# Optimization experiments

Measured on AMD Instinct MI355X. Metric: run time of the kernel, lower is better.

Reference implementation:

```python
import jax, jax.numpy as jnp
import numpy as np

N_OBJ, N_P, N2 = 16, 128, 2048
C, H, W = 256, 384, 384
IMG_W, IMG_H = 384.0, 384.0  # img_metas['img_shape'][:2][::-1]
SIM_THR = 0.0
LOSS_WEIGHT = 1.0
COS_EPS = 1e-8  # torch F.cosine_similarity default


def setup_inputs() -> dict:
    key = jax.random.key(0)
    k1, k2, k3, k4 = jax.random.split(key, 4)
    img_size = jnp.array([IMG_W, IMG_H], jnp.float32)
    point_set_1 = jax.random.uniform(k1, (N_OBJ, N_P, 2), jnp.float32) * img_size
    point_set_2 = jax.random.uniform(k2, (N_OBJ, N2, 2), jnp.float32) * img_size
    key_points = jax.random.uniform(k3, (N_OBJ * N_P, 2), jnp.float32) * img_size
    feats = jax.random.normal(k4, (1, C, H, W), jnp.float32)
    return {"point_set_1": point_set_1, "point_set_2": point_set_2,
            "feats": feats, "key_points": key_points}


def _grid_sample(img, pts01):
    # img: [C,H,W]; pts01: [P,2] (x,y) in [0,1]. Bilinear, align_corners=False,
    # zero padding -- matches mmcv point_sample / torch grid_sample.
    Ci, Hi, Wi = img.shape
    g = 2.0 * pts01 - 1.0
    x = ((g[:, 0] + 1.0) * Wi - 1.0) * 0.5
    y = ((g[:, 1] + 1.0) * Hi - 1.0) * 0.5
    x0 = jnp.floor(x)
    y0 = jnp.floor(y)
    wx1 = x - x0
    wy1 = y - y0

    def tap(xi, yi, wgt):
        valid = (xi >= 0) & (xi < Wi) & (yi >= 0) & (yi < Hi)
        xc = jnp.clip(xi, 0, Wi - 1).astype(jnp.int32)
        yc = jnp.clip(yi, 0, Hi - 1).astype(jnp.int32)
        return img[:, yc, xc] * (wgt * valid)[None, :]  # [C,P]

    return (tap(x0, y0, (1 - wx1) * (1 - wy1))
            + tap(x0 + 1, y0, wx1 * (1 - wy1))
            + tap(x0, y0 + 1, (1 - wx1) * wy1)
            + tap(x0 + 1, y0 + 1, wx1 * wy1))  # [C,P]


def reference(point_set_1, point_set_2, feats, key_points):
    img_size = jnp.array([IMG_W, IMG_H], feats.dtype)
    img = feats[0]  # feats.expand() reuses the same map for every object

    # feats_set_1: [n_obj, n_p, C]; feats_set_2: [n_obj, n2, C]
    f1 = _grid_sample(img, key_points / img_size).T.reshape(N_OBJ, N_P, C)
    f2 = _grid_sample(img, (point_set_2 / img_size).reshape(-1, 2)).T.reshape(N_OBJ, N2, C)

    # cosine similarity over channel dim (norms clamped to eps like torch)
    n1 = jnp.maximum(jnp.linalg.norm(f1, axis=-1), COS_EPS)  # [O,P]
    n2 = jnp.maximum(jnp.linalg.norm(f2, axis=-1), COS_EPS)  # [O,N2]
    sims = jnp.einsum('opc,onc->opn', f1, f2) / (n1[..., None] * n2[:, None, :])
    mask = sims >= SIM_THR  # [O,P,N2]

    # pairwise L2 distances between each key point and candidate set
    diff = point_set_1[:, :, None, :] - point_set_2[:, None, :, :]
    d = jnp.linalg.norm(diff, axis=-1)  # [O,P,N2]

    cnt = mask.sum(-1)  # [O,P]
    has = cnt > 0
    dmin = jnp.min(jnp.where(mask, d, jnp.inf), axis=-1)
    dmean = jnp.sum(jnp.where(mask, d, 0.0), axis=-1) / jnp.maximum(cnt, 1)
    # chamfer of a single point vs masked set: (nearest + mean)/2, 'mean' reduction
    m = (point_set_2.sum(axis=(1, 2)) >= 0).astype(d.dtype)  # [O]
    cost = jnp.where(has, 0.5 * (dmin + dmean), 0.0) * m[:, None]  # [O,P]

    dist = (cost.sum(-1) / N_P).mean()
    return dist * LOSS_WEIGHT
```

## Files before the change

### kernel.cpp

```cpp
#include <hip/hip_runtime.h>
#include <hip/hip_bf16.h>
#include <math.h>

#define W_    384
#define H_    384
#define HW_   (384*384)
#define C_    256
#define NOBJ  16
#define NP    128
#define N2    2048
#define NF1   (NOBJ*NP)
#define NPTS  (NOBJ*NP + NOBJ*N2)
#define NG    16
#define NT    8

#define TX    63
#define TY    8
#define NTX   7
#define NTY   48
#define NTILE (NTX*NTY)
#define CAP   256
#define CCH   32
#define DXP   68
#define CST   (9*DXP)

typedef __attribute__((ext_vector_type(8))) short short8;
typedef __attribute__((ext_vector_type(4))) float f32x4;

__device__ __forceinline__ unsigned short f2bf(float v) {
    unsigned int u = __float_as_uint(v);
    u += 0x7fffu + ((u >> 16) & 1u);
    return (unsigned short)(u >> 16);
}
__device__ __forceinline__ float bf2f(unsigned short s) {
    return __uint_as_float((unsigned)s << 16);
}

__device__ __forceinline__ void patch_setup(float px, float py,
                                            int& ixb, int& iyb,
                                            float& w00, float& w01,
                                            float& w10, float& w11) {
    float x = px - 0.5f, y = py - 0.5f;
    float xf = floorf(x), yf = floorf(y);
    int ix0 = (int)xf, iy0 = (int)yf;
    float fx = x - xf, fy = y - yf;
    ixb = min(max(ix0, 0), W_ - 2);
    iyb = min(max(iy0, 0), H_ - 2);
    float wA = (ix0 < 0) ? fx : ((ix0 >= W_ - 1) ? 0.f : 1.f - fx);
    float wB = (ix0 < 0) ? 0.f : ((ix0 >= W_ - 1) ? 1.f - fx : fx);
    float uA = (iy0 < 0) ? fy : ((iy0 >= H_ - 1) ? 0.f : 1.f - fy);
    float uB = (iy0 < 0) ? 0.f : ((iy0 >= H_ - 1) ? 1.f - fy : fy);
    w00 = uA * wA; w01 = uA * wB; w10 = uB * wA; w11 = uB * wB;
}

__global__ __launch_bounds__(256) void k_bin(const float* __restrict__ kpts,
                                             const float* __restrict__ ps2,
                                             int* __restrict__ counts,
                                             float4* __restrict__ list) {
    int p = blockIdx.x * 256 + threadIdx.x;
    const float* src = (p < NF1) ? (kpts + (size_t)p * 2)
                                 : (ps2 + (size_t)(p - NF1) * 2);
    float px = src[0], py = src[1];
    int ixb, iyb; float w00, w01, w10, w11;
    patch_setup(px, py, ixb, iyb, w00, w01, w10, w11);
    int tile = (iyb >> 3) * NTX + ixb / TX;
    int slot = atomicAdd(&counts[tile], 1);
    if (slot < CAP) {
        float4 e; e.x = px; e.y = py; e.z = __int_as_float(p); e.w = 0.f;
        list[tile * CAP + slot] = e;
    }
}

__global__ __launch_bounds__(256) void k_gather(const float* __restrict__ feats,
                                                const int* __restrict__ counts,
                                                const float4* __restrict__ list,
                                                unsigned short* __restrict__ f12) {
    __shared__ unsigned short lds[CCH * CST];
    int b    = blockIdx.x;
    int tile = b >> 3;
    int cq   = b & 7;
    int ty = tile / NTX, tx = tile - ty * NTX;
    int x0 = tx * TX, y0 = ty * TY;
    int t  = threadIdx.x;
    int cb = cq * CCH;
    bool edge = (tx == NTX - 1);

    #pragma unroll
    for (int half = 0; half < 2; ++half) {
        int id  = half * 256 + t;
        int c   = id >> 4;
        int dx4 = (id & 15) * 4;
        const float* cbase = feats + (size_t)(cb + c) * HW_;
        unsigned short* ldst = &lds[c * CST + dx4];
        #pragma unroll
        for (int dy = 0; dy < 9; ++dy) {
            int yy = min(y0 + dy, H_ - 1);
            float4 v;
            if (!edge) {
                v = *(const float4*)(cbase + yy * W_ + x0 + dx4);
            } else {
                const float* rowp = cbase + yy * W_;
                v.x = rowp[min(x0 + dx4 + 0, W_ - 1)];
                v.y = rowp[min(x0 + dx4 + 1, W_ - 1)];
                v.z = rowp[min(x0 + dx4 + 2, W_ - 1)];
                v.w = rowp[min(x0 + dx4 + 3, W_ - 1)];
            }
            ushort4 pk;
            pk.x = f2bf(v.x); pk.y = f2bf(v.y); pk.z = f2bf(v.z); pk.w = f2bf(v.w);
            *(ushort4*)(ldst + dy * DXP) = pk;
        }
    }
    __syncthreads();

    int cnt  = min(counts[tile], CAP);
    int lane = t & 63, wave = t >> 6;
    int sub  = lane >> 2;
    int g    = lane & 3;

    for (int i = wave * 16 + sub; i < cnt; i += 64) {
        float4 e = list[tile * CAP + i];
        int point = __float_as_int(e.z);
        int ixb, iyb; float w00, w01, w10, w11;
        patch_setup(e.x, e.y, ixb, iyb, w00, w01, w10, w11);
        int dxb = ixb - x0, dyb = iyb - y0;

        unsigned short u[8];
        #pragma unroll
        for (int j = 0; j < 8; ++j) {
            const unsigned short* base = &lds[(g * 8 + j) * CST + dyb * DXP + dxb];
            float v = w00 * bf2f(base[0])   + w01 * bf2f(base[1])
                    + w10 * bf2f(base[DXP]) + w11 * bf2f(base[DXP + 1]);
            u[j] = f2bf(v);
        }
        uint4 pk;
        pk.x = (unsigned)u[0] | ((unsigned)u[1] << 16);
        pk.y = (unsigned)u[2] | ((unsigned)u[3] << 16);
        pk.z = (unsigned)u[4] | ((unsigned)u[5] << 16);
        pk.w = (unsigned)u[6] | ((unsigned)u[7] << 16);
        *(uint4*)(f12 + (size_t)point * C_ + cb + g * 8) = pk;
    }
}

__global__ __launch_bounds__(256) void k_simdist(const unsigned short* __restrict__ f12,
                                                 const float* __restrict__ ps1,
                                                 const float* __restrict__ ps2,
                                                 float* __restrict__ pmin,
                                                 float* __restrict__ psum,
                                                 float* __restrict__ pcnt) {
    int wid  = blockIdx.x * 4 + (threadIdx.x >> 6);
    int lane = threadIdx.x & 63;
    int ng = wid & 15;
    int pt = (wid >> 4) & 7;
    int o  = wid >> 7;
    int quad = lane >> 4, col = lane & 15;

    const short* f12s = (const short*)f12;
    const short8* aptr =
        (const short8*)(f12s + ((size_t)(o * NP + pt * 16 + col) * C_ + quad * 8));
    short8 a[8];
    #pragma unroll
    for (int kb = 0; kb < 8; ++kb) a[kb] = aptr[kb * 4];

    const float2* ps1v = (const float2*)ps1;
    const float2* ps2v = (const float2*)ps2;
    float pxr[4], pyr[4];
    #pragma unroll
    for (int r = 0; r < 4; ++r) {
        float2 pc = ps1v[o * NP + pt * 16 + quad * 4 + r];
        pxr[r] = pc.x; pyr[r] = pc.y;
    }

    float mn[4] = {INFINITY, INFINITY, INFINITY, INFINITY};
    float sm[4] = {0.f, 0.f, 0.f, 0.f};
    float ct[4] = {0.f, 0.f, 0.f, 0.f};

    for (int t = 0; t < NT; ++t) {
        int nbase = ng * 128 + t * 16;
        const short8* bptr =
            (const short8*)(f12s + ((size_t)(NF1 + o * N2 + nbase + col) * C_ + quad * 8));
        f32x4 acc = {0.f, 0.f, 0.f, 0.f};
        #pragma unroll
        for (int kb = 0; kb < 8; ++kb)
            acc = __builtin_amdgcn_mfma_f32_16x16x32_bf16(a[kb], bptr[kb * 4], acc, 0, 0, 0);

        float2 nc = ps2v[o * N2 + nbase + col];
        #pragma unroll
        for (int r = 0; r < 4; ++r) {
            if (acc[r] >= 0.f) {
                float dx = pxr[r] - nc.x, dy = pyr[r] - nc.y;
                float d  = sqrtf(dx * dx + dy * dy);
                mn[r] = fminf(mn[r], d); sm[r] += d; ct[r] += 1.f;
            }
        }
    }

    #pragma unroll
    for (int r = 0; r < 4; ++r) {
        #pragma unroll
        for (int off = 1; off < 16; off <<= 1) {
            mn[r] = fminf(mn[r], __shfl_xor(mn[r], off, 16));
            sm[r] += __shfl_xor(sm[r], off, 16);
            ct[r] += __shfl_xor(ct[r], off, 16);
        }
    }
    if (col == 0) {
        #pragma unroll
        for (int r = 0; r < 4; ++r) {
            int p   = pt * 16 + quad * 4 + r;
            int idx = (o * NP + p) * NG + ng;
            pmin[idx] = mn[r]; psum[idx] = sm[r]; pcnt[idx] = ct[r];
        }
    }
}

__global__ __launch_bounds__(1024) void k_final(const float* __restrict__ pmin,
                                                const float* __restrict__ psum,
                                                const float* __restrict__ pcnt,
                                                float* __restrict__ out) {
    int t = threadIdx.x;
    float tot = 0.f;
    for (int pair = t; pair < NOBJ * NP; pair += 1024) {
        int base = pair * NG;
        const float4* pm = (const float4*)(pmin + base);
        const float4* ps = (const float4*)(psum + base);
        const float4* pc = (const float4*)(pcnt + base);
        float mn = INFINITY, sm = 0.f, ct = 0.f;
        #pragma unroll
        for (int g4 = 0; g4 < 4; ++g4) {
            float4 a = pm[g4], bq = ps[g4], c = pc[g4];
            mn = fminf(mn, fminf(fminf(a.x, a.y), fminf(a.z, a.w)));
            sm += bq.x + bq.y + bq.z + bq.w;
            ct += c.x + c.y + c.z + c.w;
        }
        if (ct > 0.f) tot += 0.5f * (mn + sm / ct);
    }
    #pragma unroll
    for (int off = 32; off; off >>= 1) tot += __shfl_xor(tot, off, 64);
    __shared__ float wsum[16];
    if ((t & 63) == 0) wsum[t >> 6] = tot;
    __syncthreads();
    if (t < 64) {
        float v = (t < 16) ? wsum[t] : 0.f;
        #pragma unroll
        for (int off = 8; off; off >>= 1) v += __shfl_xor(v, off, 16);
        if (t == 0) out[0] = v * (1.0f / (NOBJ * NP));
    }
}

extern "C" void kernel_launch(void* const* d_in, const int* in_sizes, int n_in,
                              void* d_out, int out_size, void* d_ws, size_t ws_size,
                              hipStream_t stream) {
    const float* ps1   = (const float*)d_in[0];
    const float* ps2   = (const float*)d_in[1];
    const float* feats = (const float*)d_in[2];
    const float* kpts  = (const float*)d_in[3];
    float* out = (float*)d_out;

    const size_t sz_f12  = (size_t)NPTS * C_ * sizeof(unsigned short);
    const size_t sz_part = (size_t)NOBJ * NP * NG * sizeof(float);
    const size_t sz_cnt  = (size_t)NTILE * sizeof(int);
    const size_t sz_cnt_pad = 4096;

    char* ws = (char*)d_ws;
    unsigned short* f12 = (unsigned short*)ws;
    float*  pmin = (float*) (ws + sz_f12);
    float*  psum = (float*) (ws + sz_f12 + sz_part);
    float*  pcnt = (float*) (ws + sz_f12 + 2 * sz_part);
    int*    cnts = (int*)   (ws + sz_f12 + 3 * sz_part);
    float4* list = (float4*)(ws + sz_f12 + 3 * sz_part + sz_cnt_pad);

    hipMemsetAsync(cnts, 0, sz_cnt, stream);
    k_bin<<<NPTS / 256, 256, 0, stream>>>(kpts, ps2, cnts, list);
    k_gather<<<NTILE * 8, 256, 0, stream>>>(feats, cnts, list, f12);
    k_simdist<<<NOBJ * 8 * NG / 4, 256, 0, stream>>>(f12, ps1, ps2, pmin, psum, pcnt);
    k_final<<<1, 1024, 0, stream>>>(pmin, psum, pcnt, out);
}
```

Baseline: 290.7 us.

## Restructure tile gather: smaller channel chunks, fp32 LDS, batched row loads

The tile-staging gather kernel now handles 16 channels per block instead of 32, which doubles the grid and sets launch bounds for 4 blocks per CU. Each thread issues all nine float4 row loads into registers before writing any of them to LDS. Tiles are stored in LDS as fp32, so the bf16 round-trip during staging and the bf16 decode during interpolation both go away. The edge-column special case is replaced by a clamped linear index that may read into the next row; those columns are never used in interpolation. The intent is more memory-level parallelism on the feature-map read, in exchange for narrower 8-byte output stores and more blocks re-reading the halo rows.

Result: faster. 276.5 us (-4.9%).

```diff
diff --git a/kernel.cpp b/kernel.cpp
--- a/kernel.cpp
+++ b/kernel.cpp
@@ -20,9 +20,7 @@
 #define NTY   48
 #define NTILE (NTX*NTY)
 #define CAP   256
-#define CCH   32
-#define DXP   68
-#define CST   (9*DXP)
+#define CCH   16
 
 typedef __attribute__((ext_vector_type(8))) short short8;
 typedef __attribute__((ext_vector_type(4))) float f32x4;
@@ -31,9 +29,6 @@
     unsigned int u = __float_as_uint(v);
     u += 0x7fffu + ((u >> 16) & 1u);
     return (unsigned short)(u >> 16);
-}
-__device__ __forceinline__ float bf2f(unsigned short s) {
-    return __uint_as_float((unsigned)s << 16);
 }
 
 __device__ __forceinline__ void patch_setup(float px, float py,
@@ -71,44 +66,36 @@
     }
 }
 
-__global__ __launch_bounds__(256) void k_gather(const float* __restrict__ feats,
-                                                const int* __restrict__ counts,
-                                                const float4* __restrict__ list,
-                                                unsigned short* __restrict__ f12) {
-    __shared__ unsigned short lds[CCH * CST];
+__global__ __launch_bounds__(256, 4) void k_gather(const float* __restrict__ feats,
+                                                   const int* __restrict__ counts,
+                                                   const float4* __restrict__ list,
+                                                   unsigned short* __restrict__ f12) {
+    __shared__ float lds[9 * 16 * 64];
     int b    = blockIdx.x;
-    int tile = b >> 3;
-    int cq   = b & 7;
+    int tile = b >> 4;
+    int cq   = b & 15;
+    int cb   = cq * CCH;
     int ty = tile / NTX, tx = tile - ty * NTX;
     int x0 = tx * TX, y0 = ty * TY;
     int t  = threadIdx.x;
-    int cb = cq * CCH;
-    bool edge = (tx == NTX - 1);
-
-    #pragma unroll
-    for (int half = 0; half < 2; ++half) {
-        int id  = half * 256 + t;
-        int c   = id >> 4;
-        int dx4 = (id & 15) * 4;
-        const float* cbase = feats + (size_t)(cb + c) * HW_;
-        unsigned short* ldst = &lds[c * CST + dx4];
+
+    {
+        int c   = t >> 4;
+        int dx4 = (t & 15) * 4;
+        size_t cgbase = (size_t)(cb + c) * HW_ + x0 + dx4;
+        const size_t LIM = (size_t)HW_ * C_ - 4;
+        float4 r[9];
         #pragma unroll
         for (int dy = 0; dy < 9; ++dy) {
             int yy = min(y0 + dy, H_ - 1);
-            float4 v;
-            if (!edge) {
-                v = *(const float4*)(cbase + yy * W_ + x0 + dx4);
-            } else {
-                const float* rowp = cbase + yy * W_;
-                v.x = rowp[min(x0 + dx4 + 0, W_ - 1)];
-                v.y = rowp[min(x0 + dx4 + 1, W_ - 1)];
-                v.z = rowp[min(x0 + dx4 + 2, W_ - 1)];
-                v.w = rowp[min(x0 + dx4 + 3, W_ - 1)];
-            }
-            ushort4 pk;
-            pk.x = f2bf(v.x); pk.y = f2bf(v.y); pk.z = f2bf(v.z); pk.w = f2bf(v.w);
-            *(ushort4*)(ldst + dy * DXP) = pk;
-        }
+            size_t gidx = cgbase + (size_t)yy * W_;
+            gidx = gidx > LIM ? LIM : gidx;
+            r[dy] = *(const float4*)(feats + gidx);
+        }
+        float* ldst = &lds[c * 64 + dx4];
+        #pragma unroll
+        for (int dy = 0; dy < 9; ++dy)
+            *(float4*)(ldst + dy * 1024) = r[dy];
     }
     __syncthreads();
 
@@ -123,21 +110,20 @@
         int ixb, iyb; float w00, w01, w10, w11;
         patch_setup(e.x, e.y, ixb, iyb, w00, w01, w10, w11);
         int dxb = ixb - x0, dyb = iyb - y0;
-
-        unsigned short u[8];
-        #pragma unroll
-        for (int j = 0; j < 8; ++j) {
-            const unsigned short* base = &lds[(g * 8 + j) * CST + dyb * DXP + dxb];
-            float v = w00 * bf2f(base[0])   + w01 * bf2f(base[1])
-                    + w10 * bf2f(base[DXP]) + w11 * bf2f(base[DXP + 1]);
+        int base0 = dyb * 1024 + (g * 4) * 64 + dxb;
+
+        unsigned short u[4];
+        #pragma unroll
+        for (int j = 0; j < 4; ++j) {
+            int bj = base0 + j * 64;
+            float v = w00 * lds[bj]        + w01 * lds[bj + 1]
+                    + w10 * lds[bj + 1024] + w11 * lds[bj + 1025];
             u[j] = f2bf(v);
         }
-        uint4 pk;
+        uint2 pk;
         pk.x = (unsigned)u[0] | ((unsigned)u[1] << 16);
         pk.y = (unsigned)u[2] | ((unsigned)u[3] << 16);
-        pk.z = (unsigned)u[4] | ((unsigned)u[5] << 16);
-        pk.w = (unsigned)u[6] | ((unsigned)u[7] << 16);
-        *(uint4*)(f12 + (size_t)point * C_ + cb + g * 8) = pk;
+        *(uint2*)(f12 + (size_t)point * C_ + cb + g * 4) = pk;
     }
 }
 
@@ -271,7 +257,7 @@
 
     hipMemsetAsync(cnts, 0, sz_cnt, stream);
     k_bin<<<NPTS / 256, 256, 0, stream>>>(kpts, ps2, cnts, list);
-    k_gather<<<NTILE * 8, 256, 0, stream>>>(feats, cnts, list, f12);
+    k_gather<<<NTILE * 16, 256, 0, stream>>>(feats, cnts, list, f12);
     k_simdist<<<NOBJ * 8 * NG / 4, 256, 0, stream>>>(f12, ps1, ps2, pmin, psum, pcnt);
     k_final<<<1, 1024, 0, stream>>>(pmin, psum, pcnt, out);
 }
```
